# Performance work log

Measured on AMD Instinct MI355X. Metric: run time of the kernel, lower is better.

Reference implementation:

```python
import jax, jax.numpy as jnp
import numpy as np

B, N, C = 4, 1370, 1024
H, DH = 16, C // 16
N_ROPE = 1369  # patch tokens covered by RoPE (prefix=1 CLS token)


def _rotate_half(x):
    x1, x2 = jnp.split(x, 2, axis=-1)
    return jnp.concatenate([-x2, x1], axis=-1)


def _rope_apply(x, sin, cos):
    return x * cos + _rotate_half(x) * sin


def setup_inputs() -> dict:
    key = jax.random.key(0)
    ks = jax.random.split(key, 7)
    return {
        "x": jax.random.normal(ks[0], (B, N, C), dtype=jnp.float32),
        "sin": jax.random.normal(ks[1], (N_ROPE, DH), dtype=jnp.float32),
        "cos": jax.random.normal(ks[2], (N_ROPE, DH), dtype=jnp.float32),
        "w_qkv": jax.random.normal(ks[3], (C, 3 * C), dtype=jnp.float32) * (C ** -0.5),
        "b_qkv": jax.random.normal(ks[4], (3 * C,), dtype=jnp.float32) * 0.02,
        "w_proj": jax.random.normal(ks[5], (C, C), dtype=jnp.float32) * (C ** -0.5),
        "b_proj": jax.random.normal(ks[6], (C,), dtype=jnp.float32) * 0.02,
    }


def reference(x, sin, cos, w_qkv, b_qkv, w_proj, b_proj):
    b, n, c = x.shape
    # QKV projection -> [3, B, H, N, DH]
    qkv = (x @ w_qkv + b_qkv).reshape(b, n, 3, H, DH).transpose(2, 0, 3, 1, 4)
    q, k, v = qkv[0], qkv[1], qkv[2]
    # RoPE on the last N_ROPE tokens (prefix tokens, e.g. CLS, left untouched)
    prefix = n - sin.shape[-2]
    q = jnp.concatenate([q[:, :, :prefix, :], _rope_apply(q[:, :, prefix:, :], sin, cos)], axis=-2)
    k = jnp.concatenate([k[:, :, :prefix, :], _rope_apply(k[:, :, prefix:, :], sin, cos)], axis=-2)
    # Full attention
    scale = 1.0 / jnp.sqrt(jnp.asarray(DH, dtype=x.dtype))
    attn = jnp.einsum('bhqd,bhkd->bhqk', q, k) * scale
    attn = jax.nn.softmax(attn, axis=-1)
    out = jnp.einsum('bhqk,bhkd->bhqd', attn, v)
    out = out.transpose(0, 2, 1, 3).reshape(b, n, c)
    return out @ w_proj + b_proj
```

## Files before the change

kernel.cpp:

```cpp
#include <hip/hip_runtime.h>
#include <hip/hip_bf16.h>

#define B_ 4
#define N_ 1370
#define C_ 1024
#define H_ 16
#define DH_ 64
#define NR_ 1369
#define M_ (B_*N_)
#define VTS_ 1408
#define ALS 64
#define PLS 72
#define SVS 200

#define QSCALE 0.1803368801111f

typedef _Float16 f16x8  __attribute__((ext_vector_type(8)));
typedef __bf16   bf16x8 __attribute__((ext_vector_type(8)));
typedef float    f32x4  __attribute__((ext_vector_type(4)));

__device__ __forceinline__ f16x8 ld_frag_h(const unsigned short* p) {
    uint4 u = *(const uint4*)p;
    return __builtin_bit_cast(f16x8, u);
}
__device__ __forceinline__ bf16x8 ld_frag_b(const unsigned short* p) {
    uint4 u = *(const uint4*)p;
    return __builtin_bit_cast(bf16x8, u);
}
__device__ __forceinline__ unsigned short f2h(float f) {
    _Float16 h = (_Float16)f;
    return __builtin_bit_cast(unsigned short, h);
}
__device__ __forceinline__ unsigned short f2bf(float f) {
    __hip_bfloat16 h = __float2bfloat16(f);
    return __builtin_bit_cast(unsigned short, h);
}
__device__ __forceinline__ bf16x8 ones_bf() {
    uint4 u = make_uint4(0x3F803F80u, 0x3F803F80u, 0x3F803F80u, 0x3F803F80u);
    return __builtin_bit_cast(bf16x8, u);
}

__device__ __forceinline__ void load_lds16(const unsigned short* g, unsigned short* l) {
    __builtin_amdgcn_global_load_lds(
        (const __attribute__((address_space(1))) unsigned int*)g,
        (__attribute__((address_space(3))) unsigned int*)l,
        16, 0, 0);
}

#define XBLK 5480
#define WQBLK 768
#define WPBLK 256
#define VTBLK 64
__global__ __launch_bounds__(256)
void prep_k(const float* __restrict__ x, unsigned short* __restrict__ xo,
            const float* __restrict__ wq, unsigned short* __restrict__ wqt,
            const float* __restrict__ wp, unsigned short* __restrict__ wpt,
            unsigned short* __restrict__ vt)
{
    __shared__ unsigned short Th[64][68];
    int bid = blockIdx.x;
    if (bid < XBLK) {
        const int i = bid * 256 + threadIdx.x;
        float4 v = ((const float4*)x)[i];
        ushort4 h;
        h.x = f2h(v.x); h.y = f2h(v.y); h.z = f2h(v.z); h.w = f2h(v.w);
        ((ushort4*)xo)[i] = h;
        return;
    }
    bid -= XBLK;
    if (bid >= WQBLK + WPBLK) {
        const int bh = bid - (WQBLK + WPBLK);
        unsigned short* base = vt + (size_t)bh * DH_ * VTS_;
        for (int e = threadIdx.x; e < DH_ * (VTS_ - N_); e += 256) {
            const int d = e / (VTS_ - N_), t = e - d * (VTS_ - N_);
            base[(size_t)d * VTS_ + N_ + t] = 0;
        }
        return;
    }
    const float* w; unsigned short* wt; int Ncol, nb;
    if (bid < WQBLK) { w = wq; wt = wqt; Ncol = 3072; nb = 48; }
    else { bid -= WQBLK; w = wp; wt = wpt; Ncol = 1024; nb = 16; }
    const int tid = threadIdx.x, tx = tid & 15, ty = tid >> 4;
    const int n0 = (bid % nb) * 64, k0 = (bid / nb) * 64;
    #pragma unroll
    for (int i = 0; i < 4; ++i) {
        const int k = ty + i * 16;
        float4 v = *(const float4*)&w[(size_t)(k0 + k) * Ncol + n0 + tx * 4];
        Th[k][tx*4+0] = f2h(v.x); Th[k][tx*4+1] = f2h(v.y);
        Th[k][tx*4+2] = f2h(v.z); Th[k][tx*4+3] = f2h(v.w);
    }
    __syncthreads();
    #pragma unroll
    for (int i = 0; i < 4; ++i) {
        const int n = ty + i * 16;
        ushort4 o;
        o.x = Th[tx*4+0][n]; o.y = Th[tx*4+1][n]; o.z = Th[tx*4+2][n]; o.w = Th[tx*4+3][n];
        *(ushort4*)&wt[(size_t)(n0 + n) * 1024 + k0 + tx * 4] = o;
    }
}

__global__ __launch_bounds__(512, 4)
void gemm_qkv8(const unsigned short* __restrict__ A, const unsigned short* __restrict__ Bt,
               const float* __restrict__ bias,
               unsigned short* __restrict__ qb, unsigned short* __restrict__ kb,
               unsigned short* __restrict__ vt,
               const float* __restrict__ sinp, const float* __restrict__ cosp)
{
    __shared__ __align__(16) unsigned short SMEM[40960];
    unsigned short* const A_s = SMEM;
    unsigned short* const B_s = SMEM + 24576;

    const int tid = threadIdx.x;
    const int wave = tid >> 6, lane = tid & 63;
    const int quad = lane >> 4, l16 = lane & 15;

    const int id  = blockIdx.x;
    const int lid = (id & 7) * 87 + (id >> 3);
    const int mblk = lid / 24, nblk = lid - mblk * 24;
    const int m0 = mblk * 192, n0 = nblk * 128;

    const int mwave = (wave >> 1) * 48;
    const int nwave = (wave & 1) * 64;

    const int srow = lane >> 3;
    const int gseg = (lane & 7) ^ srow;

    f32x4 acc[3][4] = {};

    auto stage = [&](int kc, int buf) {
        const int kof = kc * 64;
        #pragma unroll
        for (int i = 0; i < 3; ++i) {
            const int rbase = wave * 24 + i * 8;
            int arow = m0 + rbase + srow;
            if (arow > M_ - 1) arow = M_ - 1;
            load_lds16(A + (size_t)arow * 1024 + kof + gseg * 8,
                       A_s + buf * 12288 + rbase * 64);
        }
        #pragma unroll
        for (int i = 0; i < 2; ++i) {
            const int rbase = wave * 16 + i * 8;
            const int brow = n0 + rbase + srow;
            load_lds16(Bt + (size_t)brow * 1024 + kof + gseg * 8,
                       B_s + buf * 8192 + rbase * 64);
        }
    };

    stage(0, 0);

    for (int kc = 0; kc < 16; ++kc) {
        const int cur = kc & 1;
        __syncthreads();
        if (kc + 1 < 16) stage(kc + 1, cur ^ 1);

        #pragma unroll
        for (int kh = 0; kh < 2; ++kh) {
            const int soff = (((kh * 4 + quad) ^ (l16 & 7)) << 3);
            f16x8 a[3], b[4];
            #pragma unroll
            for (int t = 0; t < 3; ++t)
                a[t] = ld_frag_h(A_s + cur * 12288 + (mwave + t * 16 + l16) * 64 + soff);
            #pragma unroll
            for (int t = 0; t < 4; ++t)
                b[t] = ld_frag_h(B_s + cur * 8192 + (nwave + t * 16 + l16) * 64 + soff);
            #pragma unroll
            for (int i = 0; i < 3; ++i)
                #pragma unroll
                for (int j = 0; j < 4; ++j)
                    acc[i][j] = __builtin_amdgcn_mfma_f32_16x16x32_f16(a[i], b[j], acc[i][j], 0, 0, 0);
        }
    }

    const int nbase = n0 + nwave;

    if (n0 >= 2048) {
        unsigned short* const Sv = SMEM;
        __syncthreads();
        #pragma unroll
        for (int i = 0; i < 3; ++i) {
            #pragma unroll
            for (int r = 0; r < 4; ++r) {
                const int tl = mwave + i * 16 + quad * 4 + r;
                #pragma unroll
                for (int j = 0; j < 4; ++j) {
                    const int c = nwave + j * 16 + l16;
                    Sv[c * SVS + tl] = f2bf(acc[i][j][r] + bias[nbase + j * 16 + l16]);
                }
            }
        }
        __syncthreads();
        const int b0 = m0 / N_;
        const int cross = (b0 + 1) * N_ - m0;
        const int hbase = n0 & 1023;
        for (int cr = 0; cr < 16; ++cr) {
            const int c = wave * 16 + cr;
            const int h = (hbase + c) >> 6;
            const int d = c & 63;
            #pragma unroll
            for (int it = 0; it < 3; ++it) {
                const int tl = it * 64 + lane;
                const int gm = m0 + tl;
                if (gm < M_) {
                    const int b = b0 + (tl >= cross ? 1 : 0);
                    const int tok = gm - b * N_;
                    vt[((size_t)((b * H_ + h) * DH_ + d)) * VTS_ + tok] = Sv[c * SVS + tl];
                }
            }
        }
        return;
    }

    const int part = nbase >> 10;
    const int h = (nbase & 1023) >> 6;
    #pragma unroll
    for (int i = 0; i < 3; ++i) {
        #pragma unroll
        for (int r = 0; r < 4; ++r) {
            const int gm = m0 + mwave + i * 16 + quad * 4 + r;
            if (gm >= M_) continue;
            const int b = gm / N_;
            const int tok = gm - b * N_;

            float val[4];
            #pragma unroll
            for (int j = 0; j < 4; ++j)
                val[j] = acc[i][j][r] + bias[nbase + j * 16 + l16];

            if (tok >= 1) {
                const float* sp = sinp + (size_t)(tok - 1) * DH_;
                const float* cp = cosp + (size_t)(tok - 1) * DH_;
                const float s0 = sp[l16],      s1 = sp[16 + l16];
                const float s2 = sp[32 + l16], s3 = sp[48 + l16];
                const float c0 = cp[l16],      c1 = cp[16 + l16];
                const float c2 = cp[32 + l16], c3 = cp[48 + l16];
                const float n0v = fmaf(val[0], c0, -val[2] * s0);
                const float n1v = fmaf(val[1], c1, -val[3] * s1);
                const float n2v = fmaf(val[2], c2,  val[0] * s2);
                const float n3v = fmaf(val[3], c3,  val[1] * s3);
                val[0] = n0v; val[1] = n1v; val[2] = n2v; val[3] = n3v;
            }

            const int bh = b * H_ + h;
            #pragma unroll
            for (int j = 0; j < 4; ++j) {
                const int d = j * 16 + l16;
                if (part == 0) qb[((size_t)bh * N_ + tok) * DH_ + d] = f2h(val[j] * QSCALE);
                else           kb[((size_t)bh * N_ + tok) * DH_ + d] = f2h(val[j]);
            }
        }
    }
}

__global__ __launch_bounds__(256)
void gemm_proj2(const unsigned short* __restrict__ A, const unsigned short* __restrict__ Bt,
                const float* __restrict__ bias, float* __restrict__ out)
{
    __shared__ __align__(16) unsigned short A_s[2][64 * 64];
    __shared__ __align__(16) unsigned short B_s[2][128 * 64];

    const int tid = threadIdx.x;
    const int wave = tid >> 6, lane = tid & 63;
    const int quad = lane >> 4, l16 = lane & 15;
    const int m0 = blockIdx.y * 64, n0 = blockIdx.x * 128;
    const int mwave = (wave & 1) * 32, nwave = (wave >> 1) * 64;

    const int srow = lane >> 3;
    const int gseg = (lane & 7) ^ srow;

    f32x4 acc[2][4] = {};

    auto stage = [&](int kc, int buf) {
        const int kof = kc * 64;
        #pragma unroll
        for (int i = 0; i < 2; ++i) {
            const int rbase = wave * 16 + i * 8;
            int arow = m0 + rbase + srow;
            if (arow > M_ - 1) arow = M_ - 1;
            load_lds16(A + (size_t)arow * 1024 + kof + gseg * 8, &A_s[buf][rbase * 64]);
        }
        #pragma unroll
        for (int i = 0; i < 4; ++i) {
            const int rbase = wave * 32 + i * 8;
            const int brow = n0 + rbase + srow;
            load_lds16(Bt + (size_t)brow * 1024 + kof + gseg * 8, &B_s[buf][rbase * 64]);
        }
    };

    stage(0, 0);

    for (int kc = 0; kc < 16; ++kc) {
        const int cur = kc & 1;
        __syncthreads();
        if (kc + 1 < 16) stage(kc + 1, cur ^ 1);

        #pragma unroll
        for (int kh = 0; kh < 2; ++kh) {
            const int soff = (((kh * 4 + quad) ^ (l16 & 7)) << 3);
            f16x8 a[2], b[4];
            #pragma unroll
            for (int t = 0; t < 2; ++t)
                a[t] = ld_frag_h(&A_s[cur][(mwave + t * 16 + l16) * 64 + soff]);
            #pragma unroll
            for (int t = 0; t < 4; ++t)
                b[t] = ld_frag_h(&B_s[cur][(nwave + t * 16 + l16) * 64 + soff]);
            #pragma unroll
            for (int i = 0; i < 2; ++i)
                #pragma unroll
                for (int j = 0; j < 4; ++j)
                    acc[i][j] = __builtin_amdgcn_mfma_f32_16x16x32_f16(a[i], b[j], acc[i][j], 0, 0, 0);
        }
    }

    #pragma unroll
    for (int i = 0; i < 2; ++i) {
        #pragma unroll
        for (int r = 0; r < 4; ++r) {
            const int gm = m0 + mwave + i * 16 + quad * 4 + r;
            if (gm >= M_) continue;
            #pragma unroll
            for (int j = 0; j < 4; ++j) {
                const int gn = n0 + nwave + j * 16 + l16;
                out[(size_t)gm * 1024 + gn] = acc[i][j][r] + bias[gn];
            }
        }
    }
}

__global__ __launch_bounds__(512, 6)
void attn_k(const unsigned short* __restrict__ q, const unsigned short* __restrict__ k,
            const unsigned short* __restrict__ vt, unsigned short* __restrict__ out)
{
    __shared__ __align__(16) unsigned short Ks[2][64 * ALS];
    __shared__ __align__(16) unsigned short Vs[2][64 * ALS];
    __shared__ __align__(16) unsigned short Ps[8 * 16 * PLS];

    const int tid  = threadIdx.x;
    const int wave = tid >> 6, lane = tid & 63;
    const int quad = lane >> 4, l16 = lane & 15;
    const int srow = lane >> 3;
    const int gseg = (lane & 7) ^ srow;

    const int id  = blockIdx.x;
    const int lid = (id & 7) * 88 + (id >> 3);
    const int bh  = lid / 11;
    const int q0  = (lid - bh * 11) * 128;

    const unsigned short* qp  = q  + (size_t)bh * N_ * DH_;
    const unsigned short* kp  = k  + (size_t)bh * N_ * DH_;
    const unsigned short* vtp = vt + (size_t)bh * DH_ * VTS_;

    f16x8 qf[2];
    {
        int qrow = q0 + wave * 16 + l16;
        if (qrow > N_ - 1) qrow = N_ - 1;
        qf[0] = ld_frag_h(qp + (size_t)qrow * DH_ + quad * 8);
        qf[1] = ld_frag_h(qp + (size_t)qrow * DH_ + 32 + quad * 8);
    }

    const bf16x8 onesv = ones_bf();
    f32x4 O[4] = {};
    f32x4 L = {};

    unsigned short* Pw = Ps + wave * 16 * PLS;
    const int so0 = ((quad)     ^ (l16 & 7)) << 3;
    const int so1 = ((4 + quad) ^ (l16 & 7)) << 3;

    auto stage = [&](int ch, int buf) {
        const int k0 = ch * 64;
        const int rbase = wave * 8;
        int krow = k0 + rbase + srow;
        if (krow > N_ - 1) krow = N_ - 1;
        load_lds16(kp + (size_t)krow * DH_ + gseg * 8, &Ks[buf][rbase * ALS]);
        load_lds16(vtp + (size_t)(rbase + srow) * VTS_ + k0 + gseg * 8, &Vs[buf][rbase * ALS]);
    };

    stage(0, 0);

    for (int ch = 0; ch < 22; ++ch) {
        const int k0 = ch * 64;
        const int cur = ch & 1;
        __syncthreads();
        if (ch + 1 < 22) stage(ch + 1, 1 - cur);

        f16x8 kf[4][2];
        #pragma unroll
        for (int t = 0; t < 4; ++t) {
            kf[t][0] = ld_frag_h(&Ks[cur][(t * 16 + l16) * ALS + so0]);
            kf[t][1] = ld_frag_h(&Ks[cur][(t * 16 + l16) * ALS + so1]);
        }
        f32x4 S[4];
        #pragma unroll
        for (int t = 0; t < 4; ++t) {
            f32x4 z = {};
            z = __builtin_amdgcn_mfma_f32_16x16x32_f16(qf[0], kf[t][0], z, 0, 0, 0);
            z = __builtin_amdgcn_mfma_f32_16x16x32_f16(qf[1], kf[t][1], z, 0, 0, 0);
            S[t] = z;
        }
        if (k0 + 64 > N_) {
            #pragma unroll
            for (int t = 0; t < 4; ++t) {
                if (k0 + t * 16 + l16 >= N_) {
                    S[t][0] = -1e30f; S[t][1] = -1e30f;
                    S[t][2] = -1e30f; S[t][3] = -1e30f;
                }
            }
        }

        #pragma unroll
        for (int t = 0; t < 4; ++t) {
            #pragma unroll
            for (int r = 0; r < 4; ++r) {
                const float p = __builtin_amdgcn_exp2f(S[t][r]);
                Pw[(quad * 4 + r) * PLS + t * 16 + l16] = f2bf(p);
            }
        }
        __builtin_amdgcn_wave_barrier();

        bf16x8 pf[2];
        pf[0] = ld_frag_b(&Pw[l16 * PLS + quad * 8]);
        pf[1] = ld_frag_b(&Pw[l16 * PLS + 32 + quad * 8]);

        bf16x8 vf[4][2];
        #pragma unroll
        for (int dt = 0; dt < 4; ++dt) {
            vf[dt][0] = ld_frag_b(&Vs[cur][(dt * 16 + l16) * ALS + so0]);
            vf[dt][1] = ld_frag_b(&Vs[cur][(dt * 16 + l16) * ALS + so1]);
        }
        L = __builtin_amdgcn_mfma_f32_16x16x32_bf16(pf[0], onesv, L, 0, 0, 0);
        L = __builtin_amdgcn_mfma_f32_16x16x32_bf16(pf[1], onesv, L, 0, 0, 0);
        #pragma unroll
        for (int dt = 0; dt < 4; ++dt) {
            O[dt] = __builtin_amdgcn_mfma_f32_16x16x32_bf16(pf[0], vf[dt][0], O[dt], 0, 0, 0);
            O[dt] = __builtin_amdgcn_mfma_f32_16x16x32_bf16(pf[1], vf[dt][1], O[dt], 0, 0, 0);
        }
    }

    const int b = bh >> 4, h = bh & 15;
    #pragma unroll
    for (int r = 0; r < 4; ++r) {
        const int qi = q0 + wave * 16 + quad * 4 + r;
        if (qi < N_) {
            const float inv = 1.0f / L[r];
            unsigned short* op = out + ((size_t)(b * N_ + qi)) * C_ + h * DH_ + l16;
            #pragma unroll
            for (int dt = 0; dt < 4; ++dt) op[dt * 16] = f2h(O[dt][r] * inv);
        }
    }
}

extern "C" void kernel_launch(void* const* d_in, const int* in_sizes, int n_in,
                              void* d_out, int out_size, void* d_ws, size_t ws_size,
                              hipStream_t stream) {
    const float* x      = (const float*)d_in[0];
    const float* sinp   = (const float*)d_in[1];
    const float* cosp   = (const float*)d_in[2];
    const float* w_qkv  = (const float*)d_in[3];
    const float* b_qkv  = (const float*)d_in[4];
    const float* w_proj = (const float*)d_in[5];
    const float* b_proj = (const float*)d_in[6];
    float* out = (float*)d_out;

    unsigned short* p = (unsigned short*)d_ws;
    const size_t xsz  = (size_t)M_ * C_;
    const size_t wqsz = (size_t)3 * C_ * C_;
    const size_t wpsz = (size_t)C_ * C_;
    const size_t hsz  = (size_t)B_ * H_ * N_ * DH_;
    const size_t vtsz = (size_t)B_ * H_ * DH_ * VTS_;
    unsigned short* x_h   = p;            p += xsz;
    unsigned short* wq_t  = p;            p += wqsz;
    unsigned short* wp_t  = p;            p += wpsz;
    unsigned short* q     = p;            p += hsz;
    unsigned short* k     = p;            p += hsz;
    unsigned short* vt    = p;            p += vtsz;
    unsigned short* attnb = p;            p += xsz;

    prep_k<<<dim3(XBLK + WQBLK + WPBLK + VTBLK), 256, 0, stream>>>(
        x, x_h, w_qkv, wq_t, w_proj, wp_t, vt);

    gemm_qkv8<<<dim3(696), 512, 0, stream>>>(
        x_h, wq_t, b_qkv, q, k, vt, sinp, cosp);

    attn_k<<<dim3(11 * B_ * H_), 512, 0, stream>>>(q, k, vt, attnb);

    gemm_proj2<<<dim3(C_ / 128, (M_ + 63) / 64), 256, 0, stream>>>(
        attnb, wp_t, b_proj, out);
}
```

Baseline: 226.1 us.

## Process two 16-row query slices per wave in attention, halve block size

Result: slower. 234.4 us (+3.6%).

```diff
diff --git a/kernel.cpp b/kernel.cpp
--- a/kernel.cpp
+++ b/kernel.cpp
@@ -326,13 +326,13 @@
     }
 }
 
-__global__ __launch_bounds__(512, 6)
+__global__ __launch_bounds__(256)
 void attn_k(const unsigned short* __restrict__ q, const unsigned short* __restrict__ k,
             const unsigned short* __restrict__ vt, unsigned short* __restrict__ out)
 {
     __shared__ __align__(16) unsigned short Ks[2][64 * ALS];
     __shared__ __align__(16) unsigned short Vs[2][64 * ALS];
-    __shared__ __align__(16) unsigned short Ps[8 * 16 * PLS];
+    __shared__ __align__(16) unsigned short Ps[4 * 32 * PLS];
 
     const int tid  = threadIdx.x;
     const int wave = tid >> 6, lane = tid & 63;
@@ -349,29 +349,33 @@
     const unsigned short* kp  = k  + (size_t)bh * N_ * DH_;
     const unsigned short* vtp = vt + (size_t)bh * DH_ * VTS_;
 
-    f16x8 qf[2];
-    {
-        int qrow = q0 + wave * 16 + l16;
+    f16x8 qf[2][2];
+    #pragma unroll
+    for (int s = 0; s < 2; ++s) {
+        int qrow = q0 + wave * 32 + s * 16 + l16;
         if (qrow > N_ - 1) qrow = N_ - 1;
-        qf[0] = ld_frag_h(qp + (size_t)qrow * DH_ + quad * 8);
-        qf[1] = ld_frag_h(qp + (size_t)qrow * DH_ + 32 + quad * 8);
+        qf[s][0] = ld_frag_h(qp + (size_t)qrow * DH_ + quad * 8);
+        qf[s][1] = ld_frag_h(qp + (size_t)qrow * DH_ + 32 + quad * 8);
     }
 
     const bf16x8 onesv = ones_bf();
-    f32x4 O[4] = {};
-    f32x4 L = {};
-
-    unsigned short* Pw = Ps + wave * 16 * PLS;
+    f32x4 O[2][4] = {};
+    f32x4 L[2] = {};
+
+    unsigned short* Pw = Ps + wave * 32 * PLS;
     const int so0 = ((quad)     ^ (l16 & 7)) << 3;
     const int so1 = ((4 + quad) ^ (l16 & 7)) << 3;
 
     auto stage = [&](int ch, int buf) {
         const int k0 = ch * 64;
-        const int rbase = wave * 8;
-        int krow = k0 + rbase + srow;
-        if (krow > N_ - 1) krow = N_ - 1;
-        load_lds16(kp + (size_t)krow * DH_ + gseg * 8, &Ks[buf][rbase * ALS]);
-        load_lds16(vtp + (size_t)(rbase + srow) * VTS_ + k0 + gseg * 8, &Vs[buf][rbase * ALS]);
+        #pragma unroll
+        for (int i = 0; i < 2; ++i) {
+            const int rbase = wave * 16 + i * 8;
+            int krow = k0 + rbase + srow;
+            if (krow > N_ - 1) krow = N_ - 1;
+            load_lds16(kp + (size_t)krow * DH_ + gseg * 8, &Ks[buf][rbase * ALS]);
+            load_lds16(vtp + (size_t)(rbase + srow) * VTS_ + k0 + gseg * 8, &Vs[buf][rbase * ALS]);
+        }
     };
 
     stage(0, 0);
@@ -388,62 +392,79 @@
             kf[t][0] = ld_frag_h(&Ks[cur][(t * 16 + l16) * ALS + so0]);
             kf[t][1] = ld_frag_h(&Ks[cur][(t * 16 + l16) * ALS + so1]);
         }
-        f32x4 S[4];
-        #pragma unroll
-        for (int t = 0; t < 4; ++t) {
-            f32x4 z = {};
-            z = __builtin_amdgcn_mfma_f32_16x16x32_f16(qf[0], kf[t][0], z, 0, 0, 0);
-            z = __builtin_amdgcn_mfma_f32_16x16x32_f16(qf[1], kf[t][1], z, 0, 0, 0);
-            S[t] = z;
+        f32x4 S[2][4];
+        #pragma unroll
+        for (int s = 0; s < 2; ++s) {
+            #pragma unroll
+            for (int t = 0; t < 4; ++t) {
+                f32x4 z = {};
+                z = __builtin_amdgcn_mfma_f32_16x16x32_f16(qf[s][0], kf[t][0], z, 0, 0, 0);
+                z = __builtin_amdgcn_mfma_f32_16x16x32_f16(qf[s][1], kf[t][1], z, 0, 0, 0);
+                S[s][t] = z;
+            }
         }
         if (k0 + 64 > N_) {
             #pragma unroll
             for (int t = 0; t < 4; ++t) {
                 if (k0 + t * 16 + l16 >= N_) {
-                    S[t][0] = -1e30f; S[t][1] = -1e30f;
-                    S[t][2] = -1e30f; S[t][3] = -1e30f;
+                    #pragma unroll
+                    for (int s = 0; s < 2; ++s) {
+                        S[s][t][0] = -1e30f; S[s][t][1] = -1e30f;
+                        S[s][t][2] = -1e30f; S[s][t][3] = -1e30f;
+                    }
                 }
             }
         }
 
         #pragma unroll
-        for (int t = 0; t < 4; ++t) {
-            #pragma unroll
-            for (int r = 0; r < 4; ++r) {
-                const float p = __builtin_amdgcn_exp2f(S[t][r]);
-                Pw[(quad * 4 + r) * PLS + t * 16 + l16] = f2bf(p);
+        for (int s = 0; s < 2; ++s) {
+            #pragma unroll
+            for (int t = 0; t < 4; ++t) {
+                #pragma unroll
+                for (int r = 0; r < 4; ++r) {
+                    const float p = __builtin_amdgcn_exp2f(S[s][t][r]);
+                    Pw[(s * 16 + quad * 4 + r) * PLS + t * 16 + l16] = f2bf(p);
+                }
             }
         }
         __builtin_amdgcn_wave_barrier();
 
-        bf16x8 pf[2];
-        pf[0] = ld_frag_b(&Pw[l16 * PLS + quad * 8]);
-        pf[1] = ld_frag_b(&Pw[l16 * PLS + 32 + quad * 8]);
-
+        bf16x8 pf[2][2];
+        #pragma unroll
+        for (int s = 0; s < 2; ++s) {
+            pf[s][0] = ld_frag_b(&Pw[(s * 16 + l16) * PLS + quad * 8]);
+            pf[s][1] = ld_frag_b(&Pw[(s * 16 + l16) * PLS + 32 + quad * 8]);
+        }
         bf16x8 vf[4][2];
         #pragma unroll
         for (int dt = 0; dt < 4; ++dt) {
             vf[dt][0] = ld_frag_b(&Vs[cur][(dt * 16 + l16) * ALS + so0]);
             vf[dt][1] = ld_frag_b(&Vs[cur][(dt * 16 + l16) * ALS + so1]);
         }
-        L = __builtin_amdgcn_mfma_f32_16x16x32_bf16(pf[0], onesv, L, 0, 0, 0);
-        L = __builtin_amdgcn_mfma_f32_16x16x32_bf16(pf[1], onesv, L, 0, 0, 0);
-        #pragma unroll
-        for (int dt = 0; dt < 4; ++dt) {
-            O[dt] = __builtin_amdgcn_mfma_f32_16x16x32_bf16(pf[0], vf[dt][0], O[dt], 0, 0, 0);
-            O[dt] = __builtin_amdgcn_mfma_f32_16x16x32_bf16(pf[1], vf[dt][1], O[dt], 0, 0, 0);
+        #pragma unroll
+        for (int s = 0; s < 2; ++s) {
+            L[s] = __builtin_amdgcn_mfma_f32_16x16x32_bf16(pf[s][0], onesv, L[s], 0, 0, 0);
+            L[s] = __builtin_amdgcn_mfma_f32_16x16x32_bf16(pf[s][1], onesv, L[s], 0, 0, 0);
+            #pragma unroll
+            for (int dt = 0; dt < 4; ++dt) {
+                O[s][dt] = __builtin_amdgcn_mfma_f32_16x16x32_bf16(pf[s][0], vf[dt][0], O[s][dt], 0, 0, 0);
+                O[s][dt] = __builtin_amdgcn_mfma_f32_16x16x32_bf16(pf[s][1], vf[dt][1], O[s][dt], 0, 0, 0);
+            }
         }
     }
 
     const int b = bh >> 4, h = bh & 15;
     #pragma unroll
-    for (int r = 0; r < 4; ++r) {
-        const int qi = q0 + wave * 16 + quad * 4 + r;
-        if (qi < N_) {
-            const float inv = 1.0f / L[r];
-            unsigned short* op = out + ((size_t)(b * N_ + qi)) * C_ + h * DH_ + l16;
-            #pragma unroll
-            for (int dt = 0; dt < 4; ++dt) op[dt * 16] = f2h(O[dt][r] * inv);
+    for (int s = 0; s < 2; ++s) {
+        #pragma unroll
+        for (int r = 0; r < 4; ++r) {
+            const int qi = q0 + wave * 32 + s * 16 + quad * 4 + r;
+            if (qi < N_) {
+                const float inv = 1.0f / L[s][r];
+                unsigned short* op = out + ((size_t)(b * N_ + qi)) * C_ + h * DH_ + l16;
+                #pragma unroll
+                for (int dt = 0; dt < 4; ++dt) op[dt * 16] = f2h(O[s][dt][r] * inv);
+            }
         }
     }
 }
@@ -480,7 +501,7 @@
     gemm_qkv8<<<dim3(696), 512, 0, stream>>>(
         x_h, wq_t, b_qkv, q, k, vt, sinp, cosp);
 
-    attn_k<<<dim3(11 * B_ * H_), 512, 0, stream>>>(q, k, vt, attnb);
+    attn_k<<<dim3(11 * B_ * H_), 256, 0, stream>>>(q, k, vt, attnb);
 
     gemm_proj2<<<dim3(C_ / 128, (M_ + 63) / 64), 256, 0, stream>>>(
         attnb, wp_t, b_proj, out);
```

## Split attention key chunks across wave pairs and halve query tile per block

Applied to the files above, without the earlier changes.

Measured after the change: 223.7 us. No clear change (-1.1%).

```diff
diff --git a/kernel.cpp b/kernel.cpp
--- a/kernel.cpp
+++ b/kernel.cpp
@@ -330,20 +330,23 @@
 void attn_k(const unsigned short* __restrict__ q, const unsigned short* __restrict__ k,
             const unsigned short* __restrict__ vt, unsigned short* __restrict__ out)
 {
-    __shared__ __align__(16) unsigned short Ks[2][64 * ALS];
-    __shared__ __align__(16) unsigned short Vs[2][64 * ALS];
-    __shared__ __align__(16) unsigned short Ps[8 * 16 * PLS];
+    __shared__ __align__(16) unsigned short SMEM[20992];
+    unsigned short* const Ks = SMEM;
+    unsigned short* const Vs = SMEM + 8192;
+    unsigned short* const Ps = SMEM + 16384;
 
     const int tid  = threadIdx.x;
     const int wave = tid >> 6, lane = tid & 63;
+    const int qg   = wave >> 1;
+    const int kh   = wave & 1;
     const int quad = lane >> 4, l16 = lane & 15;
     const int srow = lane >> 3;
     const int gseg = (lane & 7) ^ srow;
 
     const int id  = blockIdx.x;
-    const int lid = (id & 7) * 88 + (id >> 3);
-    const int bh  = lid / 11;
-    const int q0  = (lid - bh * 11) * 128;
+    const int lid = (id & 7) * 176 + (id >> 3);
+    const int bh  = lid / 22;
+    const int q0  = (lid - bh * 22) * 64;
 
     const unsigned short* qp  = q  + (size_t)bh * N_ * DH_;
     const unsigned short* kp  = k  + (size_t)bh * N_ * DH_;
@@ -351,7 +354,7 @@
 
     f16x8 qf[2];
     {
-        int qrow = q0 + wave * 16 + l16;
+        int qrow = q0 + qg * 16 + l16;
         if (qrow > N_ - 1) qrow = N_ - 1;
         qf[0] = ld_frag_h(qp + (size_t)qrow * DH_ + quad * 8);
         qf[1] = ld_frag_h(qp + (size_t)qrow * DH_ + 32 + quad * 8);
@@ -361,17 +364,18 @@
     f32x4 O[4] = {};
     f32x4 L = {};
 
-    unsigned short* Pw = Ps + wave * 16 * PLS;
+    unsigned short* Pw = Ps + qg * 16 * PLS;
     const int so0 = ((quad)     ^ (l16 & 7)) << 3;
     const int so1 = ((4 + quad) ^ (l16 & 7)) << 3;
+    const int svo = ((kh * 4 + quad) ^ (l16 & 7)) << 3;
 
     auto stage = [&](int ch, int buf) {
         const int k0 = ch * 64;
         const int rbase = wave * 8;
         int krow = k0 + rbase + srow;
         if (krow > N_ - 1) krow = N_ - 1;
-        load_lds16(kp + (size_t)krow * DH_ + gseg * 8, &Ks[buf][rbase * ALS]);
-        load_lds16(vtp + (size_t)(rbase + srow) * VTS_ + k0 + gseg * 8, &Vs[buf][rbase * ALS]);
+        load_lds16(kp + (size_t)krow * DH_ + gseg * 8, Ks + buf * 4096 + rbase * ALS);
+        load_lds16(vtp + (size_t)(rbase + srow) * VTS_ + k0 + gseg * 8, Vs + buf * 4096 + rbase * ALS);
     };
 
     stage(0, 0);
@@ -382,15 +386,15 @@
         __syncthreads();
         if (ch + 1 < 22) stage(ch + 1, 1 - cur);
 
-        f16x8 kf[4][2];
-        #pragma unroll
-        for (int t = 0; t < 4; ++t) {
-            kf[t][0] = ld_frag_h(&Ks[cur][(t * 16 + l16) * ALS + so0]);
-            kf[t][1] = ld_frag_h(&Ks[cur][(t * 16 + l16) * ALS + so1]);
-        }
-        f32x4 S[4];
-        #pragma unroll
-        for (int t = 0; t < 4; ++t) {
+        f16x8 kf[2][2];
+        #pragma unroll
+        for (int t = 0; t < 2; ++t) {
+            kf[t][0] = ld_frag_h(Ks + cur * 4096 + (kh * 32 + t * 16 + l16) * ALS + so0);
+            kf[t][1] = ld_frag_h(Ks + cur * 4096 + (kh * 32 + t * 16 + l16) * ALS + so1);
+        }
+        f32x4 S[2];
+        #pragma unroll
+        for (int t = 0; t < 2; ++t) {
             f32x4 z = {};
             z = __builtin_amdgcn_mfma_f32_16x16x32_f16(qf[0], kf[t][0], z, 0, 0, 0);
             z = __builtin_amdgcn_mfma_f32_16x16x32_f16(qf[1], kf[t][1], z, 0, 0, 0);
@@ -398,8 +402,8 @@
         }
         if (k0 + 64 > N_) {
             #pragma unroll
-            for (int t = 0; t < 4; ++t) {
-                if (k0 + t * 16 + l16 >= N_) {
+            for (int t = 0; t < 2; ++t) {
+                if (k0 + kh * 32 + t * 16 + l16 >= N_) {
                     S[t][0] = -1e30f; S[t][1] = -1e30f;
                     S[t][2] = -1e30f; S[t][3] = -1e30f;
                 }
@@ -407,43 +411,59 @@
         }
 
         #pragma unroll
-        for (int t = 0; t < 4; ++t) {
+        for (int t = 0; t < 2; ++t) {
             #pragma unroll
             for (int r = 0; r < 4; ++r) {
                 const float p = __builtin_amdgcn_exp2f(S[t][r]);
-                Pw[(quad * 4 + r) * PLS + t * 16 + l16] = f2bf(p);
+                Pw[(quad * 4 + r) * PLS + kh * 32 + t * 16 + l16] = f2bf(p);
             }
         }
         __builtin_amdgcn_wave_barrier();
 
-        bf16x8 pf[2];
-        pf[0] = ld_frag_b(&Pw[l16 * PLS + quad * 8]);
-        pf[1] = ld_frag_b(&Pw[l16 * PLS + 32 + quad * 8]);
-
-        bf16x8 vf[4][2];
-        #pragma unroll
-        for (int dt = 0; dt < 4; ++dt) {
-            vf[dt][0] = ld_frag_b(&Vs[cur][(dt * 16 + l16) * ALS + so0]);
-            vf[dt][1] = ld_frag_b(&Vs[cur][(dt * 16 + l16) * ALS + so1]);
-        }
-        L = __builtin_amdgcn_mfma_f32_16x16x32_bf16(pf[0], onesv, L, 0, 0, 0);
-        L = __builtin_amdgcn_mfma_f32_16x16x32_bf16(pf[1], onesv, L, 0, 0, 0);
-        #pragma unroll
-        for (int dt = 0; dt < 4; ++dt) {
-            O[dt] = __builtin_amdgcn_mfma_f32_16x16x32_bf16(pf[0], vf[dt][0], O[dt], 0, 0, 0);
-            O[dt] = __builtin_amdgcn_mfma_f32_16x16x32_bf16(pf[1], vf[dt][1], O[dt], 0, 0, 0);
-        }
-    }
-
-    const int b = bh >> 4, h = bh & 15;
-    #pragma unroll
-    for (int r = 0; r < 4; ++r) {
-        const int qi = q0 + wave * 16 + quad * 4 + r;
-        if (qi < N_) {
-            const float inv = 1.0f / L[r];
-            unsigned short* op = out + ((size_t)(b * N_ + qi)) * C_ + h * DH_ + l16;
-            #pragma unroll
-            for (int dt = 0; dt < 4; ++dt) op[dt * 16] = f2h(O[dt][r] * inv);
+        bf16x8 pf = ld_frag_b(&Pw[l16 * PLS + kh * 32 + quad * 8]);
+
+        bf16x8 vf[4];
+        #pragma unroll
+        for (int dt = 0; dt < 4; ++dt)
+            vf[dt] = ld_frag_b(Vs + cur * 4096 + (dt * 16 + l16) * ALS + svo);
+
+        L = __builtin_amdgcn_mfma_f32_16x16x32_bf16(pf, onesv, L, 0, 0, 0);
+        #pragma unroll
+        for (int dt = 0; dt < 4; ++dt)
+            O[dt] = __builtin_amdgcn_mfma_f32_16x16x32_bf16(pf, vf[dt], O[dt], 0, 0, 0);
+    }
+
+    __syncthreads();
+    float* const OL = (float*)SMEM;
+    if (kh) {
+        float* dst = OL + (qg * 64 + lane) * 21;
+        #pragma unroll
+        for (int dt = 0; dt < 4; ++dt)
+            #pragma unroll
+            for (int r = 0; r < 4; ++r) dst[dt * 4 + r] = O[dt][r];
+        #pragma unroll
+        for (int r = 0; r < 4; ++r) dst[16 + r] = L[r];
+    }
+    __syncthreads();
+    if (!kh) {
+        const float* src = OL + (qg * 64 + lane) * 21;
+        #pragma unroll
+        for (int dt = 0; dt < 4; ++dt)
+            #pragma unroll
+            for (int r = 0; r < 4; ++r) O[dt][r] += src[dt * 4 + r];
+        #pragma unroll
+        for (int r = 0; r < 4; ++r) L[r] += src[16 + r];
+
+        const int b = bh >> 4, h = bh & 15;
+        #pragma unroll
+        for (int r = 0; r < 4; ++r) {
+            const int qi = q0 + qg * 16 + quad * 4 + r;
+            if (qi < N_) {
+                const float inv = 1.0f / L[r];
+                unsigned short* op = out + ((size_t)(b * N_ + qi)) * C_ + h * DH_ + l16;
+                #pragma unroll
+                for (int dt = 0; dt < 4; ++dt) op[dt * 16] = f2h(O[dt][r] * inv);
+            }
         }
     }
 }
@@ -480,7 +500,7 @@
     gemm_qkv8<<<dim3(696), 512, 0, stream>>>(
         x_h, wq_t, b_qkv, q, k, vt, sinp, cosp);
 
-    attn_k<<<dim3(11 * B_ * H_), 512, 0, stream>>>(q, k, vt, attnb);
+    attn_k<<<dim3(22 * B_ * H_), 512, 0, stream>>>(q, k, vt, attnb);
 
     gemm_proj2<<<dim3(C_ / 128, (M_ + 63) / 64), 256, 0, stream>>>(
         attnb, wp_t, b_proj, out);
```
